# Performance work log

Measured on AMD Instinct MI355X. Metric: run time of the kernel, lower is better.

## Reference

```python
import jax, jax.numpy as jnp
import numpy as np

D_MODEL, D_K, D_V, NUM_BLOCKS = 1024, 128, 128, 4


def setup_inputs() -> dict:
    key = jax.random.key(0)
    ks = jax.random.split(key, 7)
    B, L = 4, 4096
    s = 1.0 / np.sqrt(D_MODEL)
    return {
        "x": jax.random.normal(ks[0], (B, L, D_MODEL), dtype=jnp.float32),
        "Wq": jax.random.normal(ks[1], (D_K, D_MODEL), dtype=jnp.float32) * s,
        "bq": jnp.zeros((D_K,), dtype=jnp.float32),
        "Wk": jax.random.normal(ks[2], (D_K, D_MODEL), dtype=jnp.float32) * s,
        "bk": jnp.zeros((D_K,), dtype=jnp.float32),
        "Wv": jax.random.normal(ks[3], (D_V, D_MODEL), dtype=jnp.float32) * s,
        "bv": jnp.zeros((D_V,), dtype=jnp.float32),
        "block_idx": 0,
    }


def reference(x, Wq, bq, Wk, bk, Wv, bv, block_idx):
    # Linear projections (torch Linear: y = x W^T + b)
    Q = jnp.einsum("bld,kd->blk", x, Wq) + bq  # [B, L, d_k]
    K = jnp.einsum("bld,kd->blk", x, Wk) + bk  # [B, L, d_k]
    V = jnp.einsum("bld,vd->blv", x, Wv) + bv  # [B, L, d_v]
    scale = 1.0 / np.sqrt(D_K)
    scores = jnp.einsum("blk,bmk->blm", Q, K) * scale  # [B, L, L]
    attn = jax.nn.softmax(scores, axis=-1)
    # The original loops NUM_BLOCKS times over identical K_remote=K, V_remote=V
    # and accumulates; this equals NUM_BLOCKS * (attn @ V).
    output = jnp.float32(NUM_BLOCKS) * jnp.einsum("blm,bmv->blv", attn, V)
    return (output, K, V)
```

## Files before the change

### kernel.cpp

```cpp
#include <hip/hip_runtime.h>

#define B_   4
#define L_   4096
#define DM_  1024
#define DK_  128
#define NSPLIT 4
#define OUT_K_OFF 2097152
#define OUT_V_OFF 4194304

typedef __attribute__((ext_vector_type(4))) float f32x4;
typedef __attribute__((ext_vector_type(8))) short short8;

__device__ __forceinline__ unsigned short f2bf(float f) {
  union { float f; unsigned int u; } v; v.f = f;
  unsigned int u = v.u;
  u += 0x7FFFu + ((u >> 16) & 1u);
  return (unsigned short)(u >> 16);
}
__device__ __forceinline__ float bf2f(unsigned short u) {
  union { unsigned int i; float f; } v; v.i = ((unsigned int)u) << 16; return v.f;
}

#define ASYNC16(gsrc, ldst)                                                          \
  __builtin_amdgcn_global_load_lds(                                                  \
      (const __attribute__((address_space(1))) unsigned int*)(gsrc),                 \
      (__attribute__((address_space(3))) unsigned int*)(ldst), 16, 0, 0)

#define MFMA16(a, b, c) __builtin_amdgcn_mfma_f32_16x16x32_bf16((a), (b), (c), 0, 0, 0)
#define VMCNT0() asm volatile("s_waitcnt vmcnt(0)" ::: "memory")

__global__ __launch_bounds__(256) void cvt_kernel(const float* __restrict__ s,
                                                  unsigned short* __restrict__ d,
                                                  int n8) {
  int i = blockIdx.x * 256 + threadIdx.x;
  if (i >= n8) return;
  const f32x4* p = (const f32x4*)(s + (size_t)i * 8);
  f32x4 a = p[0], b = p[1];
  short8 r;
  r[0] = (short)f2bf(a[0]); r[1] = (short)f2bf(a[1]);
  r[2] = (short)f2bf(a[2]); r[3] = (short)f2bf(a[3]);
  r[4] = (short)f2bf(b[0]); r[5] = (short)f2bf(b[1]);
  r[6] = (short)f2bf(b[2]); r[7] = (short)f2bf(b[3]);
  *(short8*)(d + (size_t)i * 8) = r;
}

__global__ __launch_bounds__(256) void cvtw_kernel(const float* __restrict__ Wq,
                                                   const float* __restrict__ Wk,
                                                   const float* __restrict__ Wv,
                                                   unsigned short* __restrict__ wb) {
  const float* s = (blockIdx.y == 0) ? Wq : (blockIdx.y == 1) ? Wk : Wv;
  unsigned short* d = wb + (size_t)blockIdx.y * (DK_ * DM_);
  int i = blockIdx.x * 256 + threadIdx.x;
  const f32x4* p = (const f32x4*)(s + (size_t)i * 8);
  f32x4 a = p[0], b = p[1];
  short8 r;
  r[0] = (short)f2bf(a[0]); r[1] = (short)f2bf(a[1]);
  r[2] = (short)f2bf(a[2]); r[3] = (short)f2bf(a[3]);
  r[4] = (short)f2bf(b[0]); r[5] = (short)f2bf(b[1]);
  r[6] = (short)f2bf(b[2]); r[7] = (short)f2bf(b[3]);
  *(short8*)(d + (size_t)i * 8) = r;
}

__global__ __launch_bounds__(256) void proj_kernel(
    const unsigned short* __restrict__ xb,
    const unsigned short* __restrict__ wb,
    const float* __restrict__ bias_q, const float* __restrict__ bias_k,
    const float* __restrict__ bias_v,
    unsigned short* __restrict__ qb,
    unsigned short* __restrict__ kb,
    unsigned short* __restrict__ vt,
    float* __restrict__ out) {
  __shared__ __align__(16) char smem[49152];

  const int tid  = threadIdx.x;
  const int w    = tid >> 6;
  const int lane = tid & 63;
  const int lo4  = lane & 15, hi4 = lane >> 4;
  const int wm   = w >> 1, wn = w & 1;
  const int mt   = blockIdx.x;
  const int wt   = blockIdx.y;
  const int r0   = mt * 64;
  const unsigned short* wsrc = wb + (size_t)wt * (DK_ * DM_);

  auto stage = [&](int buf, int kt) {
    const int kc0 = kt * 64;
    char* Al = smem + buf * 24576;
    char* Bl = Al + 8192;
#pragma unroll
    for (int j = 0; j < 2; ++j) {
      unsigned int o   = (unsigned)(w * 2048 + j * 1024 + lane * 16);
      unsigned int row = o >> 7;
      unsigned int cl  = ((o >> 4) & 7) ^ (row & 7);
      ASYNC16(xb + ((size_t)(r0 + row) * DM_ + kc0 + cl * 8), Al + w * 2048 + j * 1024);
    }
#pragma unroll
    for (int j = 0; j < 4; ++j) {
      unsigned int o   = (unsigned)(w * 4096 + j * 1024 + lane * 16);
      unsigned int row = o >> 7;
      unsigned int cl  = ((o >> 4) & 7) ^ (row & 7);
      ASYNC16(wsrc + ((size_t)row * DM_ + kc0 + cl * 8), Bl + w * 4096 + j * 1024);
    }
  };

  f32x4 acc[2][4];
#pragma unroll
  for (int i = 0; i < 2; i++)
#pragma unroll
    for (int j = 0; j < 4; j++) acc[i][j] = (f32x4){0.f, 0.f, 0.f, 0.f};

  stage(0, 0);
  VMCNT0();
  __builtin_amdgcn_s_barrier();
  int cur = 0;

  for (int kt = 0; kt < 16; ++kt) {
    if (kt < 15) stage(cur ^ 1, kt + 1);
    char* Alds = smem + cur * 24576;
    char* Blds = Alds + 8192;
#pragma unroll
    for (int kk = 0; kk < 2; ++kk) {
      short8 af[2], bf[4];
#pragma unroll
      for (int mi = 0; mi < 2; mi++) {
        int row = wm * 32 + mi * 16 + lo4;
        int c   = kk * 4 + hi4;
        af[mi]  = *(const short8*)(Alds + row * 128 + (((c ^ (row & 7))) << 4));
      }
#pragma unroll
      for (int ni = 0; ni < 4; ni++) {
        int col = wn * 64 + ni * 16 + lo4;
        int c   = kk * 4 + hi4;
        bf[ni]  = *(const short8*)(Blds + col * 128 + (((c ^ (col & 7))) << 4));
      }
#pragma unroll
      for (int mi = 0; mi < 2; mi++)
#pragma unroll
        for (int ni = 0; ni < 4; ni++)
          acc[mi][ni] = MFMA16(af[mi], bf[ni], acc[mi][ni]);
    }
    VMCNT0();
    __builtin_amdgcn_s_barrier();
    cur ^= 1;
  }

  const float* bias = (wt == 0) ? bias_q : (wt == 1) ? bias_k : bias_v;
  float bv4[4];
#pragma unroll
  for (int ni = 0; ni < 4; ni++) bv4[ni] = bias[wn * 64 + ni * 16 + lo4];

  const int b_idx = r0 >> 12;
  const int l0    = r0 & 4095;

  if (wt != 2) {
    unsigned short* dstb = (wt == 0) ? qb : kb;
#pragma unroll
    for (int mi = 0; mi < 2; mi++)
#pragma unroll
      for (int ni = 0; ni < 4; ni++)
#pragma unroll
        for (int reg = 0; reg < 4; reg++) {
          int r   = wm * 32 + mi * 16 + hi4 * 4 + reg;
          int c   = wn * 64 + ni * 16 + lo4;
          float v = acc[mi][ni][reg] + bv4[ni];
          dstb[(size_t)(r0 + r) * DK_ + c] = f2bf(v);
          if (wt == 1) out[OUT_K_OFF + (size_t)(r0 + r) * DK_ + c] = v;
        }
  } else {
    char* T = smem;
#pragma unroll
    for (int mi = 0; mi < 2; mi++)
#pragma unroll
      for (int ni = 0; ni < 4; ni++)
#pragma unroll
        for (int reg = 0; reg < 4; reg++) {
          int r   = wm * 32 + mi * 16 + hi4 * 4 + reg;
          int c   = wn * 64 + ni * 16 + lo4;
          float v = acc[mi][ni][reg] + bv4[ni];
          out[OUT_V_OFF + (size_t)(r0 + r) * DK_ + c] = v;
          *(unsigned short*)(T + c * 144 + r * 2) = f2bf(v);
        }
    __syncthreads();
#pragma unroll
    for (int i = 0; i < 4; ++i) {
      int q = tid + i * 256;
      int d = q >> 3, lg = q & 7;
      short8 s8 = *(const short8*)(T + d * 144 + lg * 16);
      *(short8*)(vt + ((size_t)(b_idx * DK_ + d) * L_ + l0 + lg * 8)) = s8;
    }
  }
}

__global__ __launch_bounds__(256, 4) void attn_kernel(
    const unsigned short* __restrict__ qb, const unsigned short* __restrict__ kb,
    const unsigned short* __restrict__ vt,
    unsigned short* __restrict__ Opart,
    float* __restrict__ ml) {
  __shared__ __align__(16) char smem[37376];

  const int tid  = threadIdx.x;
  const int w    = tid >> 6;
  const int lane = tid & 63;
  const int lo4  = lane & 15, hi4 = lane >> 4;
  char* Plds = smem + 32768 + w * 1152;

  const int qt = blockIdx.x;
  const int b  = blockIdx.y;
  const int sp = blockIdx.z;
  const int tlo = sp * 32, thi = tlo + 32;

  unsigned int kkey[2], koff[2], vd_[2], voff[2];
#pragma unroll
  for (int i = 0; i < 2; ++i) {
    unsigned int c = i * 256 + w * 64 + lane;
    unsigned int key = c >> 4, cs = c & 15;
    kkey[i] = key;
    koff[i] = (cs ^ (key & 7)) * 8;
    unsigned int d = c >> 2, c2 = c & 3;
    vd_[i]  = d;
    voff[i] = (c2 ^ ((d >> 1) & 3)) * 8;
  }
  const unsigned short* kbase = kb + (size_t)b * L_ * DK_;
  const unsigned short* vbase = vt + (size_t)b * DK_ * L_;

  unsigned int kaddr[2][4];
#pragma unroll
  for (int st = 0; st < 2; st++) {
    unsigned int key = st * 16 + lo4;
#pragma unroll
    for (int kc = 0; kc < 4; kc++) {
      unsigned int cc = kc * 4 + hi4;
      kaddr[st][kc] = key * 256 + ((cc ^ (key & 7)) << 4);
    }
  }
  unsigned int vaddr[8];
#pragma unroll
  for (int dt = 0; dt < 8; dt++) {
    unsigned int d = dt * 16 + lo4;
    vaddr[dt] = d * 64 + ((hi4 ^ ((d >> 1) & 3)) << 4);
  }

  auto stage = [&](int buf, int t) {
    char* Kd = smem + buf * 8192;
    char* Vd = smem + 16384 + buf * 8192;
#pragma unroll
    for (int i = 0; i < 2; ++i) {
      ASYNC16(kbase + ((size_t)(t * 32 + kkey[i]) * DK_ + koff[i]),
              Kd + i * 4096 + w * 1024);
      ASYNC16(vbase + ((size_t)vd_[i] * L_ + t * 32 + voff[i]),
              Vd + i * 4096 + w * 1024);
    }
  };

  short8 aq[4];
  {
    const unsigned short* qp =
        qb + ((size_t)(b * L_ + qt * 64 + w * 16 + lo4) * DK_ + hi4 * 8);
#pragma unroll
    for (int kc = 0; kc < 4; kc++) aq[kc] = *(const short8*)(qp + kc * 32);
  }

  f32x4 o_acc[8];
#pragma unroll
  for (int dt = 0; dt < 8; dt++) o_acc[dt] = (f32x4){0.f, 0.f, 0.f, 0.f};
  float ls[4] = {0.f, 0.f, 0.f, 0.f};
  const float SC = 0.08838834764831845f * 1.4426950408889634f;

  stage(0, tlo);
  VMCNT0();
  __builtin_amdgcn_s_barrier();
  int cur = 0;

  for (int t = tlo; t < thi; ++t) {
    if (t + 1 < thi) stage(cur ^ 1, t + 1);
    const char* Kl = smem + cur * 8192;
    const char* Vl = smem + 16384 + cur * 8192;

    f32x4 s[2];
    s[0] = (f32x4){0.f, 0.f, 0.f, 0.f};
    s[1] = (f32x4){0.f, 0.f, 0.f, 0.f};
#pragma unroll
    for (int st = 0; st < 2; st++)
#pragma unroll
      for (int kc = 0; kc < 4; kc++)
        s[st] = MFMA16(aq[kc], *(const short8*)(Kl + kaddr[st][kc]), s[st]);

#pragma unroll
    for (int reg = 0; reg < 4; reg++) {
      int r = hi4 * 4 + reg;
      float p0 = exp2f(fmaf(s[0][reg], SC, -16.f));
      float p1 = exp2f(fmaf(s[1][reg], SC, -16.f));
      ls[reg] += p0 + p1;
      *(unsigned short*)(Plds + r * 72 + lo4 * 2)      = f2bf(p0);
      *(unsigned short*)(Plds + r * 72 + 32 + lo4 * 2) = f2bf(p1);
    }

    {
      short8 pa = *(const short8*)(Plds + lo4 * 72 + hi4 * 16);
#pragma unroll
      for (int dt = 0; dt < 8; dt++)
        o_acc[dt] = MFMA16(pa, *(const short8*)(Vl + vaddr[dt]), o_acc[dt]);
    }

    VMCNT0();
    __builtin_amdgcn_s_barrier();
    cur ^= 1;
  }

  float lt[4];
#pragma unroll
  for (int reg = 0; reg < 4; reg++) {
    float t = ls[reg];
    t += __shfl_xor(t, 1);
    t += __shfl_xor(t, 2);
    t += __shfl_xor(t, 4);
    t += __shfl_xor(t, 8);
    lt[reg] = t;
  }
  const size_t rowbase = (size_t)(sp * B_ + b) * L_ + qt * 64 + w * 16;
  if (lo4 == 0) {
#pragma unroll
    for (int reg = 0; reg < 4; reg++) {
      size_t idx = rowbase + hi4 * 4 + reg;
      ml[idx * 2 + 0] = 16.0f;
      ml[idx * 2 + 1] = lt[reg];
    }
  }
#pragma unroll
  for (int dt = 0; dt < 8; dt++)
#pragma unroll
    for (int reg = 0; reg < 4; reg++)
      Opart[(rowbase + hi4 * 4 + reg) * 128 + dt * 16 + lo4] = f2bf(o_acc[dt][reg]);
}

__global__ __launch_bounds__(256) void combine_kernel(
    const unsigned short* __restrict__ Opart, const float* __restrict__ ml,
    float* __restrict__ out) {
  const int qt = blockIdx.x, b = blockIdx.y, tid = threadIdx.x;
#pragma unroll
  for (int i = 0; i < 4; ++i) {
    int idx = i * 256 + tid;
    int row = idx >> 4, cg = idx & 15;
    size_t grow = (size_t)b * L_ + qt * 64 + row;
    float ms[NSPLIT], lv[NSPLIT], M = -__builtin_inff();
#pragma unroll
    for (int s = 0; s < NSPLIT; s++) {
      size_t p = ((size_t)s * B_ * L_ + grow) * 2;
      ms[s] = ml[p]; lv[s] = ml[p + 1];
      M = fmaxf(M, ms[s]);
    }
    float acc[8] = {0.f, 0.f, 0.f, 0.f, 0.f, 0.f, 0.f, 0.f};
    float lsum = 0.f;
#pragma unroll
    for (int s = 0; s < NSPLIT; s++) {
      float wgt = exp2f(ms[s] - M);
      lsum += lv[s] * wgt;
      short8 v = *(const short8*)&Opart[((size_t)(s * B_ + b) * L_ + qt * 64 + row) * 128 + cg * 8];
#pragma unroll
      for (int j = 0; j < 8; j++) acc[j] += bf2f((unsigned short)v[j]) * wgt;
    }
    float sc = 4.0f / lsum;
    f32x4 o0 = {acc[0] * sc, acc[1] * sc, acc[2] * sc, acc[3] * sc};
    f32x4 o1 = {acc[4] * sc, acc[5] * sc, acc[6] * sc, acc[7] * sc};
    float* dst = out + grow * 128 + cg * 8;
    *(f32x4*)dst = o0;
    *(f32x4*)(dst + 4) = o1;
  }
}

extern "C" void kernel_launch(void* const* d_in, const int* in_sizes, int n_in,
                              void* d_out, int out_size, void* d_ws, size_t ws_size,
                              hipStream_t stream) {
  const float* x  = (const float*)d_in[0];
  const float* Wq = (const float*)d_in[1];
  const float* bq = (const float*)d_in[2];
  const float* Wk = (const float*)d_in[3];
  const float* bk = (const float*)d_in[4];
  const float* Wv = (const float*)d_in[5];
  const float* bv = (const float*)d_in[6];
  float* out = (float*)d_out;

  unsigned short* xb = (unsigned short*)d_ws;
  unsigned short* wb = xb + (size_t)B_ * L_ * DM_;
  unsigned short* qb = wb + (size_t)3 * DK_ * DM_;
  unsigned short* kb = qb + (size_t)B_ * L_ * DK_;
  unsigned short* vt = kb + (size_t)B_ * L_ * DK_;
  unsigned short* Opart = xb;
  float* ml = (float*)(xb + (size_t)NSPLIT * B_ * L_ * DK_);

  cvt_kernel<<<(B_ * L_ * DM_) / 8 / 256, 256, 0, stream>>>(x, xb, (B_ * L_ * DM_) / 8);
  cvtw_kernel<<<dim3(64, 3), 256, 0, stream>>>(Wq, Wk, Wv, wb);

  proj_kernel<<<dim3(256, 3), 256, 0, stream>>>(xb, wb, bq, bk, bv, qb, kb, vt, out);
  attn_kernel<<<dim3(64, B_, NSPLIT), 256, 0, stream>>>(qb, kb, vt, Opart, ml);
  combine_kernel<<<dim3(64, B_), 256, 0, stream>>>(Opart, ml, out);
}
```

Baseline: 199.9 us.

## Transpose QK^T MFMA operands, pack P with cvt_pk_bf16, merge conversion kernels

```diff
diff --git a/kernel.cpp b/kernel.cpp
--- a/kernel.cpp
+++ b/kernel.cpp
@@ -20,6 +20,11 @@
 __device__ __forceinline__ float bf2f(unsigned short u) {
   union { unsigned int i; float f; } v; v.i = ((unsigned int)u) << 16; return v.f;
 }
+__device__ __forceinline__ unsigned int cvt_pk_bf16(float lo, float hi) {
+  unsigned int r;
+  asm("v_cvt_pk_bf16_f32 %0, %1, %2" : "=v"(r) : "v"(lo), "v"(hi));
+  return r;
+}
 
 #define ASYNC16(gsrc, ldst)                                                          \
   __builtin_amdgcn_global_load_lds(                                                  \
@@ -29,28 +34,22 @@
 #define MFMA16(a, b, c) __builtin_amdgcn_mfma_f32_16x16x32_bf16((a), (b), (c), 0, 0, 0)
 #define VMCNT0() asm volatile("s_waitcnt vmcnt(0)" ::: "memory")
 
-__global__ __launch_bounds__(256) void cvt_kernel(const float* __restrict__ s,
-                                                  unsigned short* __restrict__ d,
-                                                  int n8) {
-  int i = blockIdx.x * 256 + threadIdx.x;
-  if (i >= n8) return;
-  const f32x4* p = (const f32x4*)(s + (size_t)i * 8);
-  f32x4 a = p[0], b = p[1];
-  short8 r;
-  r[0] = (short)f2bf(a[0]); r[1] = (short)f2bf(a[1]);
-  r[2] = (short)f2bf(a[2]); r[3] = (short)f2bf(a[3]);
-  r[4] = (short)f2bf(b[0]); r[5] = (short)f2bf(b[1]);
-  r[6] = (short)f2bf(b[2]); r[7] = (short)f2bf(b[3]);
-  *(short8*)(d + (size_t)i * 8) = r;
-}
-
-__global__ __launch_bounds__(256) void cvtw_kernel(const float* __restrict__ Wq,
-                                                   const float* __restrict__ Wk,
-                                                   const float* __restrict__ Wv,
-                                                   unsigned short* __restrict__ wb) {
-  const float* s = (blockIdx.y == 0) ? Wq : (blockIdx.y == 1) ? Wk : Wv;
-  unsigned short* d = wb + (size_t)blockIdx.y * (DK_ * DM_);
-  int i = blockIdx.x * 256 + threadIdx.x;
+__global__ __launch_bounds__(256) void cvt_all_kernel(
+    const float* __restrict__ x, const float* __restrict__ Wq,
+    const float* __restrict__ Wk, const float* __restrict__ Wv,
+    unsigned short* __restrict__ xb, unsigned short* __restrict__ wb) {
+  const int bid = blockIdx.x;
+  const float* s;
+  unsigned short* d;
+  int i;
+  if (bid < 8192) {
+    s = x; d = xb; i = bid * 256 + threadIdx.x;
+  } else {
+    int wsel = (bid - 8192) >> 6;
+    s = (wsel == 0) ? Wq : (wsel == 1) ? Wk : Wv;
+    d = wb + (size_t)wsel * (DK_ * DM_);
+    i = ((bid - 8192) & 63) * 256 + threadIdx.x;
+  }
   const f32x4* p = (const f32x4*)(s + (size_t)i * 8);
   f32x4 a = p[0], b = p[1];
   short8 r;
@@ -195,13 +194,13 @@
     const unsigned short* __restrict__ vt,
     unsigned short* __restrict__ Opart,
     float* __restrict__ ml) {
-  __shared__ __align__(16) char smem[37376];
+  __shared__ __align__(16) char smem[37888];
 
   const int tid  = threadIdx.x;
   const int w    = tid >> 6;
   const int lane = tid & 63;
   const int lo4  = lane & 15, hi4 = lane >> 4;
-  char* Plds = smem + 32768 + w * 1152;
+  char* Plds = smem + 32768 + w * 1280;
 
   const int qt = blockIdx.x;
   const int b  = blockIdx.y;
@@ -262,7 +261,7 @@
   f32x4 o_acc[8];
 #pragma unroll
   for (int dt = 0; dt < 8; dt++) o_acc[dt] = (f32x4){0.f, 0.f, 0.f, 0.f};
-  float ls[4] = {0.f, 0.f, 0.f, 0.f};
+  float ls = 0.f;
   const float SC = 0.08838834764831845f * 1.4426950408889634f;
 
   stage(0, tlo);
@@ -275,27 +274,32 @@
     const char* Kl = smem + cur * 8192;
     const char* Vl = smem + 16384 + cur * 8192;
 
-    f32x4 s[2];
-    s[0] = (f32x4){0.f, 0.f, 0.f, 0.f};
-    s[1] = (f32x4){0.f, 0.f, 0.f, 0.f};
-#pragma unroll
-    for (int st = 0; st < 2; st++)
-#pragma unroll
-      for (int kc = 0; kc < 4; kc++)
-        s[st] = MFMA16(aq[kc], *(const short8*)(Kl + kaddr[st][kc]), s[st]);
-
+    f32x4 s0 = (f32x4){0.f, 0.f, 0.f, 0.f};
+    f32x4 s1 = (f32x4){0.f, 0.f, 0.f, 0.f};
+#pragma unroll
+    for (int kc = 0; kc < 4; kc++) {
+      s0 = MFMA16(*(const short8*)(Kl + kaddr[0][kc]), aq[kc], s0);
+      s1 = MFMA16(*(const short8*)(Kl + kaddr[1][kc]), aq[kc], s1);
+    }
+
+    float p[8];
 #pragma unroll
     for (int reg = 0; reg < 4; reg++) {
-      int r = hi4 * 4 + reg;
-      float p0 = exp2f(fmaf(s[0][reg], SC, -16.f));
-      float p1 = exp2f(fmaf(s[1][reg], SC, -16.f));
-      ls[reg] += p0 + p1;
-      *(unsigned short*)(Plds + r * 72 + lo4 * 2)      = f2bf(p0);
-      *(unsigned short*)(Plds + r * 72 + 32 + lo4 * 2) = f2bf(p1);
-    }
+      p[reg]     = exp2f(fmaf(s0[reg], SC, -16.f));
+      p[4 + reg] = exp2f(fmaf(s1[reg], SC, -16.f));
+    }
+    ls += ((p[0] + p[1]) + (p[2] + p[3])) + ((p[4] + p[5]) + (p[6] + p[7]));
 
     {
-      short8 pa = *(const short8*)(Plds + lo4 * 72 + hi4 * 16);
+      uint2 w0, w1;
+      w0.x = cvt_pk_bf16(p[0], p[1]);  w0.y = cvt_pk_bf16(p[2], p[3]);
+      w1.x = cvt_pk_bf16(p[4], p[5]);  w1.y = cvt_pk_bf16(p[6], p[7]);
+      *(uint2*)(Plds + lo4 * 80 + hi4 * 8)      = w0;
+      *(uint2*)(Plds + lo4 * 80 + 32 + hi4 * 8) = w1;
+    }
+
+    {
+      short8 pa = *(const short8*)(Plds + lo4 * 80 + hi4 * 16);
 #pragma unroll
       for (int dt = 0; dt < 8; dt++)
         o_acc[dt] = MFMA16(pa, *(const short8*)(Vl + vaddr[dt]), o_acc[dt]);
@@ -306,24 +310,13 @@
     cur ^= 1;
   }
 
-  float lt[4];
-#pragma unroll
-  for (int reg = 0; reg < 4; reg++) {
-    float t = ls[reg];
-    t += __shfl_xor(t, 1);
-    t += __shfl_xor(t, 2);
-    t += __shfl_xor(t, 4);
-    t += __shfl_xor(t, 8);
-    lt[reg] = t;
-  }
+  ls += __shfl_xor(ls, 16);
+  ls += __shfl_xor(ls, 32);
   const size_t rowbase = (size_t)(sp * B_ + b) * L_ + qt * 64 + w * 16;
-  if (lo4 == 0) {
-#pragma unroll
-    for (int reg = 0; reg < 4; reg++) {
-      size_t idx = rowbase + hi4 * 4 + reg;
-      ml[idx * 2 + 0] = 16.0f;
-      ml[idx * 2 + 1] = lt[reg];
-    }
+  if (hi4 == 0) {
+    size_t idx = rowbase + lo4;
+    ml[idx * 2 + 0] = 16.0f;
+    ml[idx * 2 + 1] = ls;
   }
 #pragma unroll
   for (int dt = 0; dt < 8; dt++)
@@ -387,9 +380,7 @@
   unsigned short* Opart = xb;
   float* ml = (float*)(xb + (size_t)NSPLIT * B_ * L_ * DK_);
 
-  cvt_kernel<<<(B_ * L_ * DM_) / 8 / 256, 256, 0, stream>>>(x, xb, (B_ * L_ * DM_) / 8);
-  cvtw_kernel<<<dim3(64, 3), 256, 0, stream>>>(Wq, Wk, Wv, wb);
-
+  cvt_all_kernel<<<8192 + 192, 256, 0, stream>>>(x, Wq, Wk, Wv, xb, wb);
   proj_kernel<<<dim3(256, 3), 256, 0, stream>>>(xb, wb, bq, bk, bv, qb, kb, vt, out);
   attn_kernel<<<dim3(64, B_, NSPLIT), 256, 0, stream>>>(qb, kb, vt, Opart, ml);
   combine_kernel<<<dim3(64, B_), 256, 0, stream>>>(Opart, ml, out);
```

Measured after the change: 185.3 us. 7.3% less time.
